# Performance work log

Hardware: AMD Instinct MI355X
Metric: run time of the kernel (lower is better)

The kernel has to match this reference:

```python
import jax, jax.numpy as jnp
import numpy as np

NUM_HEADS = 16

def setup_inputs() -> dict:
    key = jax.random.key(0)
    k1, k2 = jax.random.split(key)
    x = jax.random.normal(k1, (4, 4096, 1024), dtype=jnp.float32)
    # nn.Linear(dim, 3*dim, bias=False) weight: [3*dim, dim]
    w_qkv = jax.random.normal(k2, (3072, 1024), dtype=jnp.float32) * (1024 ** -0.5)
    return {"x": x, "w_qkv": w_qkv}

def reference(x, w_qkv):
    B, N, C = x.shape
    H = NUM_HEADS
    d = C // H
    # qkv projection: [B,N,3C] -> [3,B,H,N,d]
    qkv = jnp.einsum('bnc,oc->bno', x, w_qkv)
    qkv = qkv.reshape(B, N, 3, H, d).transpose(2, 0, 3, 1, 4)
    q, k, v = qkv[0], qkv[1], qkv[2]
    q = jax.nn.softmax(q, axis=-1) * (d ** -0.5)  # softmax over head_dim, then scale
    k = jax.nn.softmax(k, axis=-2)                # softmax over sequence dim
    context = jnp.einsum('bhnd,bhne->bhde', k, v)  # [B,H,d,d]
    out = jnp.einsum('bhnd,bhde->bhne', q, context)  # [B,H,N,d]
    return out
```

## Files before the change

### kernel.cpp

```cpp
#include <hip/hip_runtime.h>
#include <stdint.h>

typedef __attribute__((ext_vector_type(4))) float f32x4;
typedef __attribute__((ext_vector_type(8))) __bf16 bf16x8;
typedef unsigned short u16;

#define AS1 __attribute__((address_space(1)))
#define AS3 __attribute__((address_space(3)))

__device__ __forceinline__ u16 f2bf(float f) {
  uint32_t u = __float_as_uint(f);
  u += 0x7fffu + ((u >> 16) & 1u);
  return (u16)(u >> 16);
}
__device__ __forceinline__ float bf2f(u16 s) {
  return __uint_as_float(((uint32_t)s) << 16);
}

__device__ __forceinline__ void gload_lds16(const void* g, void* l) {
  __builtin_amdgcn_global_load_lds((const AS1 void*)g, (AS3 void*)l, 16, 0, 0);
}

__device__ __forceinline__ bf16x8 ones_bf16x8() {
  uint32_t o4[4] = {0x3F803F80u, 0x3F803F80u, 0x3F803F80u, 0x3F803F80u};
  return *(bf16x8*)o4;
}

__global__ __launch_bounds__(256) void cvt_all(const float* __restrict__ X,
                                               const float* __restrict__ W,
                                               u16* __restrict__ x16,
                                               u16* __restrict__ w16,
                                               float* __restrict__ ctxbase) {
  const int gb = blockIdx.x;
  if (gb >= 9728) {
    const int idx = (gb - 9728) * 256 + threadIdx.x;
    for (int i = idx; i < 66560; i += 1024)
      ((f32x4*)ctxbase)[i] = (f32x4){0.f, 0.f, 0.f, 0.f};
    return;
  }
  const float* src;
  u16* dst;
  int i;
  if (gb < 8192) {
    src = X; dst = x16; i = gb * 256 + threadIdx.x;
  } else {
    src = W; dst = w16; i = (gb - 8192) * 256 + threadIdx.x;
  }
  const f32x4 a = ((const f32x4*)src)[2 * i];
  const f32x4 b = ((const f32x4*)src)[2 * i + 1];
  ushort4 lo, hi;
  lo.x = f2bf(a.x); lo.y = f2bf(a.y); lo.z = f2bf(a.z); lo.w = f2bf(a.w);
  hi.x = f2bf(b.x); hi.y = f2bf(b.y); hi.z = f2bf(b.z); hi.w = f2bf(b.w);
  ((ushort4*)dst)[2 * i] = lo;
  ((ushort4*)dst)[2 * i + 1] = hi;
}

__global__ __launch_bounds__(512, 2) void qkv_gemm(const u16* __restrict__ X,
                                                   const u16* __restrict__ W,
                                                   float* __restrict__ QOUT,
                                                   u16* __restrict__ KV) {
  __shared__ __attribute__((aligned(16))) u16 lds[8 * 128 * 64];

  const int t = threadIdx.x;
  const int D = blockIdx.x;
  const int xcd = D & 7;
  const int s = D >> 3;
  const int otile = s % 12;
  const int mtile = (s / 12) * 8 + xcd;
  const int oblk = otile << 8;
  const int mblk = mtile << 8;

  const int wv = t >> 6;
  const int l = t & 63;
  const int wm = wv >> 2;
  const int wnx = wv & 3;
  const int l15 = l & 15;
  const int lq = l >> 4;
  const int sp = t & 7;

  char* ldsc = (char*)lds;

  auto stageA = [&](int tau, int h, int par) {
#pragma unroll
    for (int j = 0; j < 2; j++) {
      const int ur = (j << 6) | (t >> 3);
      const int R = ((ur >> 6) << 7) | (h << 6) | (ur & 63);
      const u16* g = X + (size_t)(mblk + R) * 1024 + (tau << 6) +
                     ((sp ^ (ur & 7)) << 3);
      gload_lds16(g, ldsc + (((par << 2) | h) << 14) + (((j << 9) | t) << 4));
    }
  };
  auto stageB = [&](int tau, int h, int par) {
#pragma unroll
    for (int j = 0; j < 2; j++) {
      const int ur = (j << 6) | (t >> 3);
      const int R = ((ur >> 5) << 6) | (h << 5) | (ur & 31);
      const u16* g = W + (size_t)(oblk + R) * 1024 + (tau << 6) +
                     ((sp ^ (ur & 7)) << 3);
      gload_lds16(g,
                  ldsc + (((par << 2) | 2 | h) << 14) + (((j << 9) | t) << 4));
    }
  };

  const int co0 = (((l >> 4) ^ (l & 7)) << 4);
  const int co1 = ((((l >> 4) | 4) ^ (l & 7)) << 4);
  const int aOff = ((wm << 6) | l15) << 7;
  const int bOff = ((wnx << 5) | l15) << 7;

  bf16x8 bA[2][4], bL[2][2], bH[2][2];
  auto loadA = [&](int h, int par) {
    const char* base = ldsc + (((par << 2) | h) << 14) + aOff;
#pragma unroll
    for (int fm = 0; fm < 4; fm++) {
      bA[0][fm] = *(const bf16x8*)(base + (fm << 11) + co0);
      bA[1][fm] = *(const bf16x8*)(base + (fm << 11) + co1);
    }
  };
  auto loadB2 = [&](int nh, int par, bf16x8(&bb)[2][2]) {
    const char* base = ldsc + (((par << 2) | 2 | nh) << 14) + bOff;
#pragma unroll
    for (int fn = 0; fn < 2; fn++) {
      bb[0][fn] = *(const bf16x8*)(base + (fn << 11) + co0);
      bb[1][fn] = *(const bf16x8*)(base + (fn << 11) + co1);
    }
  };

  f32x4 acc[8][4];
#pragma unroll
  for (int i = 0; i < 8; i++)
#pragma unroll
    for (int j = 0; j < 4; j++) acc[i][j] = (f32x4){0.f, 0.f, 0.f, 0.f};

  auto mfma16 = [&](int ah, int nh, bf16x8(&bb)[2][2]) {
#pragma unroll
    for (int fm = 0; fm < 4; fm++)
#pragma unroll
      for (int fn = 0; fn < 2; fn++)
#pragma unroll
        for (int ks = 0; ks < 2; ks++)
          acc[(ah << 2) | fm][(nh << 1) | fn] =
              __builtin_amdgcn_mfma_f32_16x16x32_bf16(
                  bA[ks][fm], bb[ks][fn], acc[(ah << 2) | fm][(nh << 1) | fn],
                  0, 0, 0);
  };

  stageA(0, 0, 0);
  stageA(0, 1, 0);
  stageB(0, 0, 0);
  stageB(0, 1, 0);
  asm volatile("s_waitcnt vmcnt(0)" ::: "memory");
  __builtin_amdgcn_s_barrier();

#pragma unroll 1
  for (int tau = 0; tau < 16; tau++) {
    const int par = tau & 1;
    loadA(0, par);
    loadB2(0, par, bL);
    if (tau < 15) {
      stageA(tau + 1, 0, par ^ 1);
      stageA(tau + 1, 1, par ^ 1);
      stageB(tau + 1, 0, par ^ 1);
      stageB(tau + 1, 1, par ^ 1);
    }
    __builtin_amdgcn_sched_barrier(0);
    __builtin_amdgcn_s_setprio(1);
    mfma16(0, 0, bL);
    __builtin_amdgcn_s_setprio(0);
    __builtin_amdgcn_sched_barrier(0);
    loadB2(1, par, bH);
    __builtin_amdgcn_sched_barrier(0);
    __builtin_amdgcn_s_setprio(1);
    mfma16(0, 1, bH);
    __builtin_amdgcn_s_setprio(0);
    __builtin_amdgcn_sched_barrier(0);
    loadA(1, par);
    __builtin_amdgcn_sched_barrier(0);
    __builtin_amdgcn_s_setprio(1);
    mfma16(1, 1, bH);
    mfma16(1, 0, bL);
    __builtin_amdgcn_s_setprio(0);
    asm volatile("s_waitcnt vmcnt(0)" ::: "memory");
    __builtin_amdgcn_s_barrier();
  }

  const bool is_q = (oblk < 1024);
  if (is_q) {
    float* LF = (float*)lds;
#pragma unroll 1
    for (int hh = 0; hh < 2; hh++) {
      __syncthreads();
      if (wm == hh) {
#pragma unroll
        for (int fm = 0; fm < 8; fm++) {
#pragma unroll
          for (int fn = 0; fn < 4; fn++) {
            const int colq = ((wnx << 2) | fn);
#pragma unroll
            for (int r = 0; r < 4; r++) {
              const int row = (fm << 4) + (lq << 2) + r;
              const int g = colq ^ lq;
              LF[(row << 8) + (g << 4) + l15] = acc[fm][fn][r];
            }
          }
        }
      }
      __syncthreads();
      const int nbase = mblk + (hh << 7);
#pragma unroll
      for (int p = 0; p < 16; p++) {
        const int u = (p << 9) + t;
        const int row = u >> 6;
        const int c = u & 63;
        const int g = (c >> 2) ^ ((row >> 2) & 3);
        const f32x4 v4 = *(const f32x4*)&LF[(row << 8) + (g << 4) + ((c & 3) << 2)];
        const int rowg = nbase + row;
        const int bq = rowg >> 12, n = rowg & 4095;
        const int head = (oblk >> 6) + (c >> 4);
        *(f32x4*)&QOUT[((((size_t)((bq << 4) + head)) << 12) + n) * 64 +
                       ((c & 15) << 2)] = v4;
      }
    }
  } else {
    u16* ks = KV + (((size_t)((mtile << 3) + (otile - 4))) << 16) + (wv << 13) +
              (l << 2);
#pragma unroll
    for (int fm = 0; fm < 8; fm++) {
#pragma unroll
      for (int fn = 0; fn < 4; fn++) {
        ushort4 sv;
        sv.x = f2bf(acc[fm][fn][0]);
        sv.y = f2bf(acc[fm][fn][1]);
        sv.z = f2bf(acc[fm][fn][2]);
        sv.w = f2bf(acc[fm][fn][3]);
        *(ushort4*)(ks + (((fm << 2) | fn) << 8)) = sv;
      }
    }
  }
}

__global__ __launch_bounds__(256) void ctx_colsum(const u16* __restrict__ KV,
                                                  float* __restrict__ ctxraw,
                                                  float* __restrict__ colsum) {
  __shared__ __attribute__((aligned(16))) u16 ekT[64 * 128];
  __shared__ __attribute__((aligned(16))) u16 evT[64 * 128];

  const int t = threadIdx.x;
  const int bh = blockIdx.y;
  const int b = bh >> 4, h = bh & 15;
  const int sgrp = blockIdx.x;
  const int w = t >> 6;
  const int l = t & 63;
  const int l15 = l & 15;
  const int lk = l >> 4;
  const int lq = (t >> 4) & 3;
  const int d_st = (w << 4) | l15;

  uint2 kr[8], vr[8];
  auto issue = [&](int it) {
    const int mt = (b << 4) + (sgrp << 2) + (it >> 1);
    const int wmb = it & 1;
    const size_t base = ((size_t)((mt << 3) + (h >> 2)) << 16) |
                        ((size_t)wmb << 15) | ((size_t)(h & 3) << 13) |
                        (size_t)(t << 2);
#pragma unroll
    for (int fm = 0; fm < 8; fm++) {
      kr[fm] = *(const uint2*)(KV + base + (fm << 10));
      vr[fm] = *(const uint2*)(KV + base + (fm << 10) + (4 << 16));
    }
  };
  auto stage = [&]() {
#pragma unroll
    for (int fm = 0; fm < 8; fm++) {
      const int c = (fm << 1) | (lq >> 1);
      const int off = (d_st << 8) + ((c ^ (d_st & 7)) << 4) + ((lq & 1) << 3);
      ushort4 es;
      es.x = f2bf(__expf(bf2f((u16)(kr[fm].x & 0xffff))));
      es.y = f2bf(__expf(bf2f((u16)(kr[fm].x >> 16))));
      es.z = f2bf(__expf(bf2f((u16)(kr[fm].y & 0xffff))));
      es.w = f2bf(__expf(bf2f((u16)(kr[fm].y >> 16))));
      *(ushort4*)((char*)ekT + off) = es;
      *(uint2*)((char*)evT + off) = vr[fm];
    }
  };

  f32x4 acc[4], acc1[4];
#pragma unroll
  for (int i = 0; i < 4; i++) {
    acc[i] = (f32x4){0.f, 0.f, 0.f, 0.f};
    acc1[i] = (f32x4){0.f, 0.f, 0.f, 0.f};
  }
  const bf16x8 ones = ones_bf16x8();
  const int eo = (w << 4) | l15;

  issue(0);
#pragma unroll 1
  for (int it = 0; it < 8; it++) {
    stage();
    if (it < 7) issue(it + 1);
    __syncthreads();
#pragma unroll
    for (int ksx = 0; ksx < 4; ksx++) {
      const bf16x8 bfrag = *(const bf16x8*)(
          (char*)evT + (eo << 8) + ((((ksx << 2) | lk) ^ (eo & 7)) << 4));
#pragma unroll
      for (int fmA = 0; fmA < 4; fmA++) {
        const int dA = (fmA << 4) | l15;
        const bf16x8 afrag = *(const bf16x8*)(
            (char*)ekT + (dA << 8) + ((((ksx << 2) | lk) ^ (dA & 7)) << 4));
        acc[fmA] = __builtin_amdgcn_mfma_f32_16x16x32_bf16(afrag, bfrag,
                                                           acc[fmA], 0, 0, 0);
        if (w == 0)
          acc1[fmA] = __builtin_amdgcn_mfma_f32_16x16x32_bf16(afrag, ones,
                                                              acc1[fmA], 0, 0, 0);
      }
    }
    __syncthreads();
  }

  float* dst = ctxraw + ((size_t)bh << 12);
#pragma unroll
  for (int fmA = 0; fmA < 4; fmA++)
#pragma unroll
    for (int r = 0; r < 4; r++) {
      const int d = (fmA << 4) + (lk << 2) + r;
      atomicAdd(&dst[(d << 6) + eo], acc[fmA][r]);
    }
  if (w == 0 && l15 == 0) {
#pragma unroll
    for (int fmA = 0; fmA < 4; fmA++)
#pragma unroll
      for (int r = 0; r < 4; r++) {
        const int d = (fmA << 4) + (lk << 2) + r;
        atomicAdd(&colsum[(bh << 6) + d], acc1[fmA][r]);
      }
  }
}

__global__ __launch_bounds__(256) void out_kernel(const float* __restrict__ ctxraw,
                                                  const float* __restrict__ colsum,
                                                  float* __restrict__ OUT) {
  __shared__ __attribute__((aligned(16))) u16 qe[256 * 64];
  __shared__ __attribute__((aligned(16))) u16 ctxT[64 * 64];

  const int t = threadIdx.x;
  const int bh = blockIdx.y;
  const int n0 = blockIdx.x << 8;
  const float* craw = ctxraw + ((size_t)bh << 12);
  float* qbase = OUT + ((size_t)bh * 4096 + n0) * 64;

#pragma unroll
  for (int p = 0; p < 4; p++) {
    const int vi = (p << 8) + t;
    const int d = vi >> 4;
    const int e4 = (vi & 15) << 2;
    const f32x4 cv = *(const f32x4*)(craw + (vi << 2));
    const float inv = 1.0f / colsum[(bh << 6) + d];
#pragma unroll
    for (int j = 0; j < 4; j++) {
      const int e = e4 + j;
      *(u16*)((char*)ctxT + (e << 7) + (((d >> 3) ^ (e & 7)) << 4) +
              ((d & 7) << 1)) = f2bf(cv[j] * inv);
    }
  }
#pragma unroll
  for (int p = 0; p < 16; p++) {
    const int idx = (p << 8) + t;
    const int row = idx >> 4;
    const int c4 = idx & 15;
    const f32x4 qv = *(const f32x4*)(qbase + (row << 6) + (c4 << 2));
    ushort4 ev;
    ev.x = f2bf(__expf(qv.x));
    ev.y = f2bf(__expf(qv.y));
    ev.z = f2bf(__expf(qv.z));
    ev.w = f2bf(__expf(qv.w));
    *(ushort4*)((char*)qe + (row << 7) + (((c4 >> 1) ^ (row & 7)) << 4) +
                ((c4 & 1) << 3)) = ev;
  }
  __syncthreads();

  const int w = t >> 6;
  const int l = t & 63;
  const int l15 = l & 15;
  const int lk = l >> 4;

  f32x4 acc[4][4], acc1[4];
#pragma unroll
  for (int i = 0; i < 4; i++) {
    acc1[i] = (f32x4){0.f, 0.f, 0.f, 0.f};
#pragma unroll
    for (int j = 0; j < 4; j++) acc[i][j] = (f32x4){0.f, 0.f, 0.f, 0.f};
  }
  const bf16x8 ones = ones_bf16x8();

#pragma unroll
  for (int ksx = 0; ksx < 2; ksx++) {
    bf16x8 bfr[4];
#pragma unroll
    for (int fn = 0; fn < 4; fn++) {
      const int e = (fn << 4) | l15;
      bfr[fn] = *(const bf16x8*)((char*)ctxT + (e << 7) +
                                 ((((ksx << 2) | lk) ^ (e & 7)) << 4));
    }
#pragma unroll
    for (int fm = 0; fm < 4; fm++) {
      const int row = (w << 6) | (fm << 4) | l15;
      const bf16x8 afr = *(const bf16x8*)(
          (char*)qe + (row << 7) + ((((ksx << 2) | lk) ^ (row & 7)) << 4));
      acc1[fm] = __builtin_amdgcn_mfma_f32_16x16x32_bf16(afr, ones, acc1[fm],
                                                         0, 0, 0);
#pragma unroll
      for (int fn = 0; fn < 4; fn++)
        acc[fm][fn] = __builtin_amdgcn_mfma_f32_16x16x32_bf16(afr, bfr[fn],
                                                              acc[fm][fn], 0, 0, 0);
    }
  }

#pragma unroll
  for (int fm = 0; fm < 4; fm++) {
#pragma unroll
    for (int r = 0; r < 4; r++) {
      const int row = (w << 6) + (fm << 4) + (lk << 2) + r;
      const float inv = 0.125f / acc1[fm][r];
#pragma unroll
      for (int fn = 0; fn < 4; fn++)
        qbase[(row << 6) + (fn << 4) + l15] = acc[fm][fn][r] * inv;
    }
  }
}

extern "C" void kernel_launch(void* const* d_in, const int* in_sizes, int n_in,
                              void* d_out, int out_size, void* d_ws, size_t ws_size,
                              hipStream_t stream) {
  const float* Xf = (const float*)d_in[0];
  const float* Wf = (const float*)d_in[1];

  u16* x16 = (u16*)d_ws;
  u16* w16 = x16 + (size_t)16384 * 1024;
  u16* KV = w16 + (size_t)3072 * 1024;
  float* ctxraw = (float*)(KV + (size_t)16384 * 2048);
  float* colsum = ctxraw + 64 * 64 * 64;
  float* QOUT = (float*)d_out;

  cvt_all<<<dim3(9732), 256, 0, stream>>>(Xf, Wf, x16, w16, ctxraw);
  qkv_gemm<<<dim3(768), 512, 0, stream>>>(x16, w16, QOUT, KV);
  ctx_colsum<<<dim3(4, 64), 256, 0, stream>>>(KV, ctxraw, colsum);
  out_kernel<<<dim3(16, 64), 256, 0, stream>>>(ctxraw, colsum, QOUT);
}
```

Before: 263.0 us.

## Store exp(Q) as bf16 from GEMM epilogue and double ctx_colsum grid

When the workspace is large enough, the QKV GEMM epilogue applies exp to Q and writes it as bf16 into a new EQ buffer, instead of writing fp32 Q into the output. out_kernel then loads the bf16 exp(Q) directly and no longer re-reads fp32 Q or recomputes exp, which halves that traffic. Separately, ctx_colsum gets twice as many blocks, each running half the loop iterations, to raise parallelism at the cost of more atomics. The fast path depends on ws_size, and if the workspace is too small the old path is kept.

```diff
diff --git a/kernel.cpp b/kernel.cpp
--- a/kernel.cpp
+++ b/kernel.cpp
@@ -58,7 +58,8 @@
 __global__ __launch_bounds__(512, 2) void qkv_gemm(const u16* __restrict__ X,
                                                    const u16* __restrict__ W,
                                                    float* __restrict__ QOUT,
-                                                   u16* __restrict__ KV) {
+                                                   u16* __restrict__ KV,
+                                                   u16* __restrict__ EQ) {
   __shared__ __attribute__((aligned(16))) u16 lds[8 * 128 * 64];
 
   const int t = threadIdx.x;
@@ -206,18 +207,36 @@
       }
       __syncthreads();
       const int nbase = mblk + (hh << 7);
-#pragma unroll
-      for (int p = 0; p < 16; p++) {
-        const int u = (p << 9) + t;
-        const int row = u >> 6;
-        const int c = u & 63;
-        const int g = (c >> 2) ^ ((row >> 2) & 3);
-        const f32x4 v4 = *(const f32x4*)&LF[(row << 8) + (g << 4) + ((c & 3) << 2)];
-        const int rowg = nbase + row;
-        const int bq = rowg >> 12, n = rowg & 4095;
-        const int head = (oblk >> 6) + (c >> 4);
-        *(f32x4*)&QOUT[((((size_t)((bq << 4) + head)) << 12) + n) * 64 +
-                       ((c & 15) << 2)] = v4;
+      if (EQ) {
+#pragma unroll
+        for (int p = 0; p < 16; p++) {
+          const int u = (p << 9) + t;
+          const int row = u >> 6;
+          const int c = u & 63;
+          const int g = (c >> 2) ^ ((row >> 2) & 3);
+          const f32x4 v4 = *(const f32x4*)&LF[(row << 8) + (g << 4) + ((c & 3) << 2)];
+          const int gc = oblk + ((c >> 4) << 6) + ((c & 15) << 2);
+          ushort4 sv;
+          sv.x = f2bf(__expf(v4.x));
+          sv.y = f2bf(__expf(v4.y));
+          sv.z = f2bf(__expf(v4.z));
+          sv.w = f2bf(__expf(v4.w));
+          *(ushort4*)(EQ + (size_t)(nbase + row) * 1024 + gc) = sv;
+        }
+      } else {
+#pragma unroll
+        for (int p = 0; p < 16; p++) {
+          const int u = (p << 9) + t;
+          const int row = u >> 6;
+          const int c = u & 63;
+          const int g = (c >> 2) ^ ((row >> 2) & 3);
+          const f32x4 v4 = *(const f32x4*)&LF[(row << 8) + (g << 4) + ((c & 3) << 2)];
+          const int rowg = nbase + row;
+          const int bq = rowg >> 12, n = rowg & 4095;
+          const int head = (oblk >> 6) + (c >> 4);
+          *(f32x4*)&QOUT[((((size_t)((bq << 4) + head)) << 12) + n) * 64 +
+                         ((c & 15) << 2)] = v4;
+        }
       }
     }
   } else {
@@ -257,7 +276,7 @@
 
   uint2 kr[8], vr[8];
   auto issue = [&](int it) {
-    const int mt = (b << 4) + (sgrp << 2) + (it >> 1);
+    const int mt = (b << 4) + (sgrp << 1) + (it >> 1);
     const int wmb = it & 1;
     const size_t base = ((size_t)((mt << 3) + (h >> 2)) << 16) |
                         ((size_t)wmb << 15) | ((size_t)(h & 3) << 13) |
@@ -294,9 +313,9 @@
 
   issue(0);
 #pragma unroll 1
-  for (int it = 0; it < 8; it++) {
+  for (int it = 0; it < 4; it++) {
     stage();
-    if (it < 7) issue(it + 1);
+    if (it < 3) issue(it + 1);
     __syncthreads();
 #pragma unroll
     for (int ksx = 0; ksx < 4; ksx++) {
@@ -338,7 +357,8 @@
 
 __global__ __launch_bounds__(256) void out_kernel(const float* __restrict__ ctxraw,
                                                   const float* __restrict__ colsum,
-                                                  float* __restrict__ OUT) {
+                                                  float* __restrict__ OUT,
+                                                  const u16* __restrict__ EQ) {
   __shared__ __attribute__((aligned(16))) u16 qe[256 * 64];
   __shared__ __attribute__((aligned(16))) u16 ctxT[64 * 64];
 
@@ -362,19 +382,33 @@
               ((d & 7) << 1)) = f2bf(cv[j] * inv);
     }
   }
-#pragma unroll
-  for (int p = 0; p < 16; p++) {
-    const int idx = (p << 8) + t;
-    const int row = idx >> 4;
-    const int c4 = idx & 15;
-    const f32x4 qv = *(const f32x4*)(qbase + (row << 6) + (c4 << 2));
-    ushort4 ev;
-    ev.x = f2bf(__expf(qv.x));
-    ev.y = f2bf(__expf(qv.y));
-    ev.z = f2bf(__expf(qv.z));
-    ev.w = f2bf(__expf(qv.w));
-    *(ushort4*)((char*)qe + (row << 7) + (((c4 >> 1) ^ (row & 7)) << 4) +
-                ((c4 & 1) << 3)) = ev;
+  if (EQ) {
+    const size_t rbase = ((size_t)(bh >> 4) << 12) + n0;
+    const int h6 = (bh & 15) << 6;
+#pragma unroll
+    for (int p = 0; p < 8; p++) {
+      const int idx = (p << 8) + t;
+      const int row = idx >> 3;
+      const int dg8 = idx & 7;
+      const uint4 ev =
+          *(const uint4*)(EQ + (rbase + row) * 1024 + h6 + (dg8 << 3));
+      *(uint4*)((char*)qe + (row << 7) + ((dg8 ^ (row & 7)) << 4)) = ev;
+    }
+  } else {
+#pragma unroll
+    for (int p = 0; p < 16; p++) {
+      const int idx = (p << 8) + t;
+      const int row = idx >> 4;
+      const int c4 = idx & 15;
+      const f32x4 qv = *(const f32x4*)(qbase + (row << 6) + (c4 << 2));
+      ushort4 ev;
+      ev.x = f2bf(__expf(qv.x));
+      ev.y = f2bf(__expf(qv.y));
+      ev.z = f2bf(__expf(qv.z));
+      ev.w = f2bf(__expf(qv.w));
+      *(ushort4*)((char*)qe + (row << 7) + (((c4 >> 1) ^ (row & 7)) << 4) +
+                  ((c4 & 1) << 3)) = ev;
+    }
   }
   __syncthreads();
 
@@ -437,12 +471,20 @@
   u16* x16 = (u16*)d_ws;
   u16* w16 = x16 + (size_t)16384 * 1024;
   u16* KV = w16 + (size_t)3072 * 1024;
-  float* ctxraw = (float*)(KV + (size_t)16384 * 2048);
+  const size_t need_eq = 141574144ull;
+  u16* EQ = nullptr;
+  float* ctxraw;
+  if (ws_size >= need_eq) {
+    EQ = KV + (size_t)16384 * 2048;
+    ctxraw = (float*)(EQ + (size_t)16384 * 1024);
+  } else {
+    ctxraw = (float*)(KV + (size_t)16384 * 2048);
+  }
   float* colsum = ctxraw + 64 * 64 * 64;
   float* QOUT = (float*)d_out;
 
   cvt_all<<<dim3(9732), 256, 0, stream>>>(Xf, Wf, x16, w16, ctxraw);
-  qkv_gemm<<<dim3(768), 512, 0, stream>>>(x16, w16, QOUT, KV);
-  ctx_colsum<<<dim3(4, 64), 256, 0, stream>>>(KV, ctxraw, colsum);
-  out_kernel<<<dim3(16, 64), 256, 0, stream>>>(ctxraw, colsum, QOUT);
-}
+  qkv_gemm<<<dim3(768), 512, 0, stream>>>(x16, w16, QOUT, KV, EQ);
+  ctx_colsum<<<dim3(8, 64), 256, 0, stream>>>(KV, ctxraw, colsum);
+  out_kernel<<<dim3(16, 64), 256, 0, stream>>>(ctxraw, colsum, QOUT, EQ);
+}
```

After: 264.0 us. No clear change (+0.4%).
